# Optimization experiments

Hardware: AMD Instinct MI355X
Metric: run time of the kernel (lower is better)

## Reference

```python
import jax, jax.numpy as jnp
import numpy as np

N_NODES = 100000
N_EDGES = 1600000
IN_FEATS = 64
OUT_FEATS = 64


def setup_inputs() -> dict:
    key = jax.random.key(0)
    k1, k2, k3, k4 = jax.random.split(key, 4)
    features = jax.random.normal(k1, (N_NODES, IN_FEATS), dtype=jnp.float32)
    src = jax.random.randint(k2, (N_EDGES,), 0, N_NODES, dtype=jnp.int32)
    dst = jax.random.randint(k3, (N_EDGES,), 0, N_NODES, dtype=jnp.int32)
    # Linear(in_feats, out_feats): W is [out, in] like torch, b is [out]
    W = jax.random.normal(k4, (OUT_FEATS, IN_FEATS), dtype=jnp.float32) * (1.0 / np.sqrt(IN_FEATS))
    b = jnp.zeros((OUT_FEATS,), dtype=jnp.float32)
    return {"features": features, "src": src, "dst": dst, "W": W, "b": b}


def reference(features, src, dst, W, b):
    # update_all(copy_src('h','m'), sum('m','h')): for each edge, message = h[src],
    # aggregated by sum at dst. Equivalent to a segment-sum scatter-add.
    msgs = features[src]  # [E, in_feats] gather
    agg = jax.ops.segment_sum(msgs, dst, num_segments=N_NODES)  # [N, in_feats]
    # NodeUpdateModule: Linear + relu (dropout=0 so no dropout path)
    h = jnp.einsum('ni,oi->no', agg, W) + b
    return jax.nn.relu(h)
```

## Files before the change

### kernel.cpp

```cpp
#include <hip/hip_runtime.h>

#define N_NODES 100000
#define N_EDGES 1600000
#define TILES 6250

#define NPB 128
#define NB 782
#define SUBS 256
#define CAP 14
#define OVF_CAP 16384
#define LOVF_CAP 512
#define LISTCAP 3712
#define GEMM_BLKS 98

typedef __attribute__((ext_vector_type(8))) short short8;
typedef __attribute__((ext_vector_type(4))) float f32x4;

static __device__ __forceinline__ unsigned short f2bf(float f) {
    unsigned int u = __float_as_uint(f);
    unsigned int r = (u + 0x7fffu + ((u >> 16) & 1u)) >> 16;
    return (unsigned short)r;
}
static __device__ __forceinline__ float bfl(unsigned int u) {
    return __uint_as_float(u << 16);
}
static __device__ __forceinline__ float bfh(unsigned int u) {
    return __uint_as_float(u & 0xffff0000u);
}

__global__ __launch_bounds__(1024) void gcn_prep(
    const float* __restrict__ feat, const float* __restrict__ W,
    unsigned int* __restrict__ g32,
    const int* __restrict__ src, const int* __restrict__ dst,
    unsigned int* __restrict__ cursor, unsigned int* __restrict__ region,
    unsigned int* __restrict__ ovf_cnt, uint2* __restrict__ ovf) {
    __shared__ unsigned int cnt[NB];
    __shared__ unsigned int data[NB][CAP];
    __shared__ uint2 lovf[LOVF_CAP];
    __shared__ unsigned int lovf_n, lovf_base;

    int tid = threadIdx.x;
    if (blockIdx.x >= SUBS) {
        int b = blockIdx.x - SUBS;
        int l = tid & 63, wv = tid >> 6;
        int r = l & 15, c = l >> 4;

        short8 bfr[4][2];
#pragma unroll
        for (int t = 0; t < 4; ++t)
#pragma unroll
            for (int s = 0; s < 2; ++s) {
                const float* wp = W + (16 * t + r) * 64 + 32 * s + c * 8;
                float4 w0 = *(const float4*)wp;
                float4 w1 = *(const float4*)(wp + 4);
                short8 f;
                f[0] = (short)f2bf(w0.x); f[1] = (short)f2bf(w0.y);
                f[2] = (short)f2bf(w0.z); f[3] = (short)f2bf(w0.w);
                f[4] = (short)f2bf(w1.x); f[5] = (short)f2bf(w1.y);
                f[6] = (short)f2bf(w1.z); f[7] = (short)f2bf(w1.w);
                bfr[t][s] = f;
            }

        int tile0 = (b * 16 + wv) * 4;
#pragma unroll
        for (int ti = 0; ti < 4; ++ti) {
            int tile = tile0 + ti;
            if (tile >= TILES) break;
            int m0 = tile * 16;
            f32x4 acc0 = {0,0,0,0}, acc1 = {0,0,0,0}, acc2 = {0,0,0,0}, acc3 = {0,0,0,0};
#pragma unroll
            for (int s = 0; s < 2; ++s) {
                const float* ap = feat + (m0 + r) * 64 + 32 * s + c * 8;
                float4 a0 = *(const float4*)ap;
                float4 a1 = *(const float4*)(ap + 4);
                short8 af;
                af[0] = (short)f2bf(a0.x); af[1] = (short)f2bf(a0.y);
                af[2] = (short)f2bf(a0.z); af[3] = (short)f2bf(a0.w);
                af[4] = (short)f2bf(a1.x); af[5] = (short)f2bf(a1.y);
                af[6] = (short)f2bf(a1.z); af[7] = (short)f2bf(a1.w);
                acc0 = __builtin_amdgcn_mfma_f32_16x16x32_bf16(af, bfr[0][s], acc0, 0, 0, 0);
                acc1 = __builtin_amdgcn_mfma_f32_16x16x32_bf16(af, bfr[1][s], acc1, 0, 0, 0);
                acc2 = __builtin_amdgcn_mfma_f32_16x16x32_bf16(af, bfr[2][s], acc2, 0, 0, 0);
                acc3 = __builtin_amdgcn_mfma_f32_16x16x32_bf16(af, bfr[3][s], acc3, 0, 0, 0);
            }
#pragma unroll
            for (int t = 0; t < 4; ++t) {
                f32x4 a = (t == 0) ? acc0 : (t == 1) ? acc1 : (t == 2) ? acc2 : acc3;
#pragma unroll
                for (int reg = 0; reg < 4; ++reg) {
                    float dv = a[reg];
                    float o = __shfl_xor(dv, 1);
                    if (!(l & 1)) {
                        int m = m0 + c * 4 + reg;
                        int n = 16 * t + r;
                        g32[(m * 64 + n) >> 1] =
                            (unsigned int)f2bf(dv) | ((unsigned int)f2bf(o) << 16);
                    }
                }
            }
        }
        return;
    }

    int sub = blockIdx.x;
    for (int i = tid; i < NB; i += 1024) cnt[i] = 0;
    if (tid == 0) lovf_n = 0;
    __syncthreads();

    int base = sub * (N_EDGES / SUBS);
    int end = base + (N_EDGES / SUBS);
    int i = base + tid;
    int s = 0, d = 0;
    if (i < end) { s = src[i]; d = dst[i]; }
    while (i < end) {
        int inext = i + 1024;
        int sn = 0, dn = 0;
        if (inext < end) { sn = src[inext]; dn = dst[inext]; }
        int bk = d >> 7;
        unsigned int c = atomicAdd(&cnt[bk], 1u);
        if (c < CAP) {
            data[bk][c] = ((unsigned int)(d & 127) << 17) | (unsigned int)s;
        } else {
            unsigned int o = atomicAdd(&lovf_n, 1u);
            if (o < LOVF_CAP) lovf[o] = make_uint2((unsigned int)s, (unsigned int)d);
        }
        i = inext; s = sn; d = dn;
    }
    __syncthreads();

    unsigned int rbase = (unsigned int)sub * NB * CAP;
    for (int idx = tid; idx < NB * CAP; idx += 1024) {
        int bk = idx / CAP, slot = idx - bk * CAP;
        unsigned int c = cnt[bk];
        if (slot < (int)(c < CAP ? c : CAP))
            region[rbase + (unsigned int)idx] = data[bk][slot];
    }
    for (int bk = tid; bk < NB; bk += 1024)
        cursor[sub * NB + bk] = cnt[bk];

    unsigned int n = lovf_n < LOVF_CAP ? lovf_n : LOVF_CAP;
    if (tid == 0) lovf_base = atomicAdd(ovf_cnt, n);
    __syncthreads();
    for (unsigned int t = tid; t < n; t += 1024) {
        unsigned int p = lovf_base + t;
        if (p < OVF_CAP) ovf[p] = lovf[t];
    }
}

__global__ __launch_bounds__(512) void gcn_gather3(
    const uint2* __restrict__ g64, const unsigned int* __restrict__ cursor,
    const unsigned int* __restrict__ region, const unsigned int* __restrict__ ovf_cnt,
    const uint2* __restrict__ ovf, const float* __restrict__ bias,
    float* __restrict__ out) {
    __shared__ unsigned int list[LISTCAP];
    __shared__ unsigned int sorted[LISTCAP];
    __shared__ unsigned int scnt[SUBS], soff[SUBS];
    __shared__ unsigned int cnt2[NPB], off2[NPB], cur2[NPB];
    __shared__ unsigned int ltot;

    int b = blockIdx.x;
    int tid = threadIdx.x;

    if (tid < SUBS) {
        unsigned int c = cursor[(unsigned)tid * NB + b];
        scnt[tid] = c < CAP ? c : CAP;
    }
    if (tid < NPB) cnt2[tid] = 0;
    __syncthreads();
    if (tid < SUBS) soff[tid] = scnt[tid];
    __syncthreads();
    for (int off = 1; off < SUBS; off <<= 1) {
        unsigned int t = 0;
        if (tid < SUBS && tid >= off) t = soff[tid - off];
        __syncthreads();
        if (tid < SUBS) soff[tid] += t;
        __syncthreads();
    }
    if (tid == 0) ltot = soff[SUBS - 1];
    __syncthreads();

    for (int idx = tid; idx < SUBS * CAP; idx += 512) {
        int s = idx / CAP, slot = idx - s * CAP;
        if (slot < (int)scnt[s])
            list[soff[s] - scnt[s] + slot] =
                __builtin_nontemporal_load(&region[((unsigned)s * NB + b) * CAP + slot]);
    }
    unsigned int oc = *ovf_cnt;
    if (oc > OVF_CAP) oc = OVF_CAP;
    for (unsigned int i = tid; i < oc; i += 512) {
        uint2 e = ovf[i];
        if ((int)(e.y >> 7) == b) {
            unsigned int p = atomicAdd(&ltot, 1u);
            if (p < LISTCAP) list[p] = ((e.y & 127u) << 17) | e.x;
        }
    }
    __syncthreads();
    unsigned int T = ltot < LISTCAP ? ltot : LISTCAP;

    for (unsigned int i = tid; i < T; i += 512)
        atomicAdd(&cnt2[list[i] >> 17], 1u);
    __syncthreads();
    if (tid < NPB) off2[tid] = cnt2[tid];
    __syncthreads();
    for (int off = 1; off < NPB; off <<= 1) {
        unsigned int t = 0;
        if (tid < NPB && tid >= off) t = off2[tid - off];
        __syncthreads();
        if (tid < NPB) off2[tid] += t;
        __syncthreads();
    }
    if (tid < NPB) cur2[tid] = off2[tid] - cnt2[tid];
    __syncthreads();
    for (unsigned int i = tid; i < T; i += 512) {
        unsigned int v = list[i];
        unsigned int p = atomicAdd(&cur2[v >> 17], 1u);
        if (p < LISTCAP) sorted[p] = v & 0x1FFFFu;
    }
    __syncthreads();

    int wv = tid >> 6, l = tid & 63, grp = l >> 4, k = l & 15;
#pragma unroll
    for (int nb = 0; nb < 4; ++nb) {
        int dl = wv * 16 + nb * 4 + grp;
        int node = b * NPB + dl;
        if (node < N_NODES) {
            unsigned int start = off2[dl] - cnt2[dl];
            int cnt = (int)cnt2[dl];
            float a0 = 0.f, a1 = 0.f, a2 = 0.f, a3 = 0.f;
#pragma unroll 8
            for (int j = 0; j < cnt; ++j) {
                unsigned int s0 = sorted[start + j];
                uint2 w = g64[s0 * 16 + k];
                a0 += bfl(w.x); a1 += bfh(w.x); a2 += bfl(w.y); a3 += bfh(w.y);
            }
            float4 b4 = *(const float4*)(bias + 4 * k);
            f32x4 o;
            o.x = fmaxf(a0 + b4.x, 0.0f);
            o.y = fmaxf(a1 + b4.y, 0.0f);
            o.z = fmaxf(a2 + b4.z, 0.0f);
            o.w = fmaxf(a3 + b4.w, 0.0f);
            __builtin_nontemporal_store(o, (f32x4*)(out + node * 64 + 4 * k));
        }
    }
}

extern "C" void kernel_launch(void* const* d_in, const int* in_sizes, int n_in,
                              void* d_out, int out_size, void* d_ws, size_t ws_size,
                              hipStream_t stream) {
    const float* features = (const float*)d_in[0];
    const int*   src      = (const int*)d_in[1];
    const int*   dst      = (const int*)d_in[2];
    const float* W        = (const float*)d_in[3];
    const float* b        = (const float*)d_in[4];
    float* out = (float*)d_out;

    unsigned int* ws     = (unsigned int*)d_ws;
    unsigned int* cursor = ws;
    unsigned int* ovfcnt = ws + 200192;
    uint2*        ovf    = (uint2*)(ws + 200256);
    unsigned int* region = ws + 233024;
    unsigned int* g32    = ws + 3035712;

    (void)hipMemsetAsync(ovfcnt, 0, 64 * sizeof(unsigned int), stream);

    gcn_prep<<<SUBS + GEMM_BLKS, 1024, 0, stream>>>(
        features, W, g32, src, dst, cursor, region, ovfcnt, ovf);
    gcn_gather3<<<NB, 512, 0, stream>>>((const uint2*)g32, cursor, region,
                                        ovfcnt, ovf, b, out);
}
```

Before: 80.64 us.

## Drop shared list buffer and prefix scan; histogram and sort directly from global

The gather kernel no longer stages edge entries in a shared-memory list after a 256-entry prefix scan over sub-bucket counts. It histograms destination slots straight from the region and overflow arrays, then reads both a second time to scatter into the sorted array. This removes one LISTCAP shared buffer and the scan barriers, which cuts LDS use and allows a launch-bounds occupancy hint of 8 blocks per CU. In exchange the region and overflow data are read twice from global or cache. The first read also stays nontemporal, so the second pass may miss in cache.

```diff
diff --git a/kernel.cpp b/kernel.cpp
--- a/kernel.cpp
+++ b/kernel.cpp
@@ -8,7 +8,7 @@
 #define NB 782
 #define SUBS 256
 #define CAP 14
-#define OVF_CAP 16384
+#define OVF_CAP 16384u
 #define LOVF_CAP 512
 #define LISTCAP 3712
 #define GEMM_BLKS 98
@@ -147,16 +147,14 @@
     }
 }
 
-__global__ __launch_bounds__(512) void gcn_gather3(
+__global__ __launch_bounds__(512, 8) void gcn_gather3(
     const uint2* __restrict__ g64, const unsigned int* __restrict__ cursor,
     const unsigned int* __restrict__ region, const unsigned int* __restrict__ ovf_cnt,
     const uint2* __restrict__ ovf, const float* __restrict__ bias,
     float* __restrict__ out) {
-    __shared__ unsigned int list[LISTCAP];
     __shared__ unsigned int sorted[LISTCAP];
-    __shared__ unsigned int scnt[SUBS], soff[SUBS];
+    __shared__ unsigned int scnt[SUBS];
     __shared__ unsigned int cnt2[NPB], off2[NPB], cur2[NPB];
-    __shared__ unsigned int ltot;
 
     int b = blockIdx.x;
     int tid = threadIdx.x;
@@ -167,39 +165,23 @@
     }
     if (tid < NPB) cnt2[tid] = 0;
     __syncthreads();
-    if (tid < SUBS) soff[tid] = scnt[tid];
-    __syncthreads();
-    for (int off = 1; off < SUBS; off <<= 1) {
-        unsigned int t = 0;
-        if (tid < SUBS && tid >= off) t = soff[tid - off];
-        __syncthreads();
-        if (tid < SUBS) soff[tid] += t;
-        __syncthreads();
-    }
-    if (tid == 0) ltot = soff[SUBS - 1];
-    __syncthreads();
 
     for (int idx = tid; idx < SUBS * CAP; idx += 512) {
         int s = idx / CAP, slot = idx - s * CAP;
-        if (slot < (int)scnt[s])
-            list[soff[s] - scnt[s] + slot] =
+        if (slot < (int)scnt[s]) {
+            unsigned int v =
                 __builtin_nontemporal_load(&region[((unsigned)s * NB + b) * CAP + slot]);
+            atomicAdd(&cnt2[v >> 17], 1u);
+        }
     }
     unsigned int oc = *ovf_cnt;
     if (oc > OVF_CAP) oc = OVF_CAP;
     for (unsigned int i = tid; i < oc; i += 512) {
         uint2 e = ovf[i];
-        if ((int)(e.y >> 7) == b) {
-            unsigned int p = atomicAdd(&ltot, 1u);
-            if (p < LISTCAP) list[p] = ((e.y & 127u) << 17) | e.x;
-        }
-    }
-    __syncthreads();
-    unsigned int T = ltot < LISTCAP ? ltot : LISTCAP;
-
-    for (unsigned int i = tid; i < T; i += 512)
-        atomicAdd(&cnt2[list[i] >> 17], 1u);
-    __syncthreads();
+        if ((int)(e.y >> 7) == b) atomicAdd(&cnt2[e.y & 127u], 1u);
+    }
+    __syncthreads();
+
     if (tid < NPB) off2[tid] = cnt2[tid];
     __syncthreads();
     for (int off = 1; off < NPB; off <<= 1) {
@@ -211,10 +193,21 @@
     }
     if (tid < NPB) cur2[tid] = off2[tid] - cnt2[tid];
     __syncthreads();
-    for (unsigned int i = tid; i < T; i += 512) {
-        unsigned int v = list[i];
-        unsigned int p = atomicAdd(&cur2[v >> 17], 1u);
-        if (p < LISTCAP) sorted[p] = v & 0x1FFFFu;
+
+    for (int idx = tid; idx < SUBS * CAP; idx += 512) {
+        int s = idx / CAP, slot = idx - s * CAP;
+        if (slot < (int)scnt[s]) {
+            unsigned int v = region[((unsigned)s * NB + b) * CAP + slot];
+            unsigned int p = atomicAdd(&cur2[v >> 17], 1u);
+            if (p < LISTCAP) sorted[p] = v & 0x1FFFFu;
+        }
+    }
+    for (unsigned int i = tid; i < oc; i += 512) {
+        uint2 e = ovf[i];
+        if ((int)(e.y >> 7) == b) {
+            unsigned int p = atomicAdd(&cur2[e.y & 127u], 1u);
+            if (p < LISTCAP) sorted[p] = e.x;
+        }
     }
     __syncthreads();
 
```

Measured after the change: 86.59 us. +7.4%, slower.
